# Performance work log

Measured on AMD Instinct MI355X. Metric: run time of the kernel, lower is better.

Reference implementation:

```python
import jax, jax.numpy as jnp
import numpy as np

NUM_NODES = 100000
EMBED_DIM = 128
NUM_RELATIONS = 64
BATCH = 512


def setup_inputs() -> dict:
    key = jax.random.key(0)
    k1, k2, k3, k4, k5 = jax.random.split(key, 5)
    u = jax.random.randint(k1, (BATCH,), 0, NUM_NODES)
    v = jax.random.randint(k2, (BATCH,), 0, NUM_NODES)
    r = jax.random.randint(k3, (BATCH,), 0, NUM_RELATIONS)
    node_embeddings = jax.random.normal(k4, (NUM_NODES, EMBED_DIM), dtype=jnp.float32)
    relation_matrices = jax.random.normal(k5, (NUM_RELATIONS, EMBED_DIM, EMBED_DIM), dtype=jnp.float32)
    return {"u": u, "v": v, "r": r,
            "node_embeddings": node_embeddings,
            "relation_matrices": relation_matrices}


def reference(u, v, r, node_embeddings, relation_matrices):
    u_embed = node_embeddings[u]            # [B, D]
    v_embed = node_embeddings[v]            # [B, D]
    rel = relation_matrices[r]              # [B, D, D] per-sample gathered matrices
    # torch.matmul([B,D], [B,D,D]) broadcasts u_embed over the relation batch -> [B_rel, B_u, D]
    score = jnp.einsum('ud,bde->bue', u_embed, rel)   # [B, B, D]
    # matmul with v_embed.T [D, B] -> [B, B, B]
    score = jnp.einsum('bue,ve->buv', score, v_embed)  # [B, B, B]
    return jax.nn.sigmoid(score)
```

## Files before the change

kernel.cpp:

```cpp
#include <hip/hip_runtime.h>


#define BATCH 512
#define DIM   128
#define NRELS 64
#define NTHR  256

typedef float floatx4 __attribute__((ext_vector_type(4)));

__device__ __forceinline__ void lds_barrier() {
    asm volatile("s_waitcnt lgkmcnt(0)" ::: "memory");
    __builtin_amdgcn_s_barrier();
    __builtin_amdgcn_sched_barrier(0);
}

__global__ __launch_bounds__(NTHR, 2)
void rad_fused_kernel(const int* __restrict__ u_idx,
                      const int* __restrict__ v_idx,
                      const int* __restrict__ r_idx,
                      const float* __restrict__ nodes,
                      const float* __restrict__ rels,
                      float* __restrict__ out)
{
    const int bid = (int)blockIdx.x;
    const int rel = ((bid & 7) << 3) | (bid >> 6);
    const int ut0 = ((bid >> 3) & 7) * 64;

    __shared__ int s_match[BATCH];
    __shared__ int s_mc;
    __shared__ __align__(16) float s_TsT[DIM * 64];
    __shared__ __align__(16) float s_buf[DIM * 64 + 16 * DIM];

    const int t  = (int)threadIdx.x;
    const int tu = t >> 4;
    const int tx = t & 15;

    if (t == 0) s_mc = 0;
    __syncthreads();
    for (int i = t; i < BATCH; i += NTHR) {
        if (r_idx[i] == rel) {
            int p = atomicAdd(&s_mc, 1);
            s_match[p] = i;
        }
    }

    float* UEsT = s_buf;
    float* Rs   = s_buf + DIM * 64;

    for (int i = t; i < 64 * (DIM / 4); i += NTHR) {
        const int row = i & 63;
        const int dc  = i >> 6;
        const float4 val = *reinterpret_cast<const float4*>(
            nodes + (size_t)u_idx[ut0 + row] * DIM + dc * 4);
        UEsT[(dc * 4 + 0) * 64 + row] = val.x;
        UEsT[(dc * 4 + 1) * 64 + row] = val.y;
        UEsT[(dc * 4 + 2) * 64 + row] = val.z;
        UEsT[(dc * 4 + 3) * 64 + row] = val.w;
    }
    __syncthreads();
    const int mc = s_mc;
    if (mc == 0) return;

    float accA[4][8];
    #pragma unroll
    for (int i = 0; i < 4; ++i)
        #pragma unroll
        for (int j = 0; j < 8; ++j) accA[i][j] = 0.f;

    const float* Rbase = rels + (size_t)rel * DIM * DIM;
    for (int dch = 0; dch < DIM / 16; ++dch) {
        for (int i = t; i < 16 * (DIM / 4); i += NTHR) {
            const int rr = i >> 5;
            const int cc = i & 31;
            *reinterpret_cast<float4*>(Rs + rr * DIM + cc * 4) =
                *reinterpret_cast<const float4*>(
                    Rbase + (size_t)(dch * 16 + rr) * DIM + cc * 4);
        }
        lds_barrier();
        #pragma unroll
        for (int dd = 0; dd < 16; ++dd) {
            const int d = dch * 16 + dd;
            const float4 a  = *reinterpret_cast<const float4*>(UEsT + d * 64 + tu * 4);
            const float4 b0 = *reinterpret_cast<const float4*>(Rs + dd * DIM + tx * 4);
            const float4 b1 = *reinterpret_cast<const float4*>(Rs + dd * DIM + 64 + tx * 4);
            const float av[4] = {a.x, a.y, a.z, a.w};
            const float bv[8] = {b0.x, b0.y, b0.z, b0.w, b1.x, b1.y, b1.z, b1.w};
            #pragma unroll
            for (int i = 0; i < 4; ++i)
                #pragma unroll
                for (int j = 0; j < 8; ++j)
                    accA[i][j] = fmaf(av[i], bv[j], accA[i][j]);
        }
        lds_barrier();
    }

    #pragma unroll
    for (int j = 0; j < 8; ++j) {
        const int e = (j < 4) ? (tx * 4 + j) : (64 + tx * 4 + (j - 4));
        #pragma unroll
        for (int i = 0; i < 4; ++i)
            s_TsT[e * 64 + tu * 4 + i] = accA[i][j];
    }

    float* VEsT = s_buf;
    for (int vt = 0; vt < BATCH / 64; ++vt) {
        lds_barrier();
        for (int i = t; i < 64 * (DIM / 4); i += NTHR) {
            const int row = i & 63;
            const int ec  = i >> 6;
            const float4 val = *reinterpret_cast<const float4*>(
                nodes + (size_t)v_idx[vt * 64 + row] * DIM + ec * 4);
            VEsT[(ec * 4 + 0) * 64 + row] = val.x;
            VEsT[(ec * 4 + 1) * 64 + row] = val.y;
            VEsT[(ec * 4 + 2) * 64 + row] = val.z;
            VEsT[(ec * 4 + 3) * 64 + row] = val.w;
        }
        lds_barrier();

        float acc[4][4];
        #pragma unroll
        for (int i = 0; i < 4; ++i)
            #pragma unroll
            for (int j = 0; j < 4; ++j) acc[i][j] = 0.f;

        #pragma unroll 8
        for (int e = 0; e < DIM; ++e) {
            const float4 a = *reinterpret_cast<const float4*>(s_TsT + e * 64 + tu * 4);
            const float4 b = *reinterpret_cast<const float4*>(VEsT  + e * 64 + tx * 4);
            const float av[4] = {a.x, a.y, a.z, a.w};
            const float bv[4] = {b.x, b.y, b.z, b.w};
            #pragma unroll
            for (int i = 0; i < 4; ++i)
                #pragma unroll
                for (int j = 0; j < 4; ++j)
                    acc[i][j] = fmaf(av[i], bv[j], acc[i][j]);
        }

        floatx4 sg[4];
        #pragma unroll
        for (int i = 0; i < 4; ++i) {
            sg[i].x = 1.f / (1.f + __expf(-acc[i][0]));
            sg[i].y = 1.f / (1.f + __expf(-acc[i][1]));
            sg[i].z = 1.f / (1.f + __expf(-acc[i][2]));
            sg[i].w = 1.f / (1.f + __expf(-acc[i][3]));
        }

        for (int m = 0; m < mc; ++m) {
            const int bb = s_match[m];
            float* obase = out + (size_t)bb * BATCH * BATCH + vt * 64 + tx * 4;
            #pragma unroll
            for (int i = 0; i < 4; ++i) {
                __builtin_nontemporal_store(
                    sg[i], reinterpret_cast<floatx4*>(
                               obase + (size_t)(ut0 + tu * 4 + i) * BATCH));
            }
        }
    }
}

extern "C" void kernel_launch(void* const* d_in, const int* in_sizes, int n_in,
                              void* d_out, int out_size, void* d_ws, size_t ws_size,
                              hipStream_t stream) {
    const int*   u_idx = (const int*)d_in[0];
    const int*   v_idx = (const int*)d_in[1];
    const int*   r_idx = (const int*)d_in[2];
    const float* nodes = (const float*)d_in[3];
    const float* rels  = (const float*)d_in[4];
    float* out = (float*)d_out;

    dim3 grid(NRELS * 8);
    dim3 block(NTHR);
    rad_fused_kernel<<<grid, block, 0, stream>>>(u_idx, v_idx, r_idx, nodes, rels, out);
}
```

Before: 142.7 us.

## Widen second-stage tile to 64x256 per block with chunked V staging

The second GEMM stage now processes two 256-wide v halves instead of eight 64-wide tiles. Each thread computes a 16x4 output tile, with the V embeddings staged in 16-column chunks. Each wave's output stores cover 16 full rows of 256 contiguous floats, which should give wider, better-coalesced writes to the large output. This also cuts the number of V reload passes. In exchange it uses a larger accumulator (64 registers), which may pressure occupancy at 2 blocks per CU, and adds more barriers per e-chunk.

```diff
diff --git a/kernel.cpp b/kernel.cpp
--- a/kernel.cpp
+++ b/kernel.cpp
@@ -15,12 +15,12 @@
 }
 
 __global__ __launch_bounds__(NTHR, 2)
-void rad_fused_kernel(const int* __restrict__ u_idx,
-                      const int* __restrict__ v_idx,
-                      const int* __restrict__ r_idx,
-                      const float* __restrict__ nodes,
-                      const float* __restrict__ rels,
-                      float* __restrict__ out)
+void rad_wide_kernel(const int* __restrict__ u_idx,
+                     const int* __restrict__ v_idx,
+                     const int* __restrict__ r_idx,
+                     const float* __restrict__ nodes,
+                     const float* __restrict__ rels,
+                     float* __restrict__ out)
 {
     const int bid = (int)blockIdx.x;
     const int rel = ((bid & 7) << 3) | (bid >> 6);
@@ -28,8 +28,8 @@
 
     __shared__ int s_match[BATCH];
     __shared__ int s_mc;
-    __shared__ __align__(16) float s_TsT[DIM * 64];
-    __shared__ __align__(16) float s_buf[DIM * 64 + 16 * DIM];
+    __shared__ __align__(16) float TsT[DIM * 64];
+    __shared__ __align__(16) float buf[DIM * 64 + 16 * DIM];
 
     const int t  = (int)threadIdx.x;
     const int tu = t >> 4;
@@ -44,8 +44,8 @@
         }
     }
 
-    float* UEsT = s_buf;
-    float* Rs   = s_buf + DIM * 64;
+    float* UEsT = buf;
+    float* Rs   = buf + DIM * 64;
 
     for (int i = t; i < 64 * (DIM / 4); i += NTHR) {
         const int row = i & 63;
@@ -99,60 +99,75 @@
         const int e = (j < 4) ? (tx * 4 + j) : (64 + tx * 4 + (j - 4));
         #pragma unroll
         for (int i = 0; i < 4; ++i)
-            s_TsT[e * 64 + tu * 4 + i] = accA[i][j];
+            TsT[e * 64 + tu * 4 + i] = accA[i][j];
     }
 
-    float* VEsT = s_buf;
-    for (int vt = 0; vt < BATCH / 64; ++vt) {
-        lds_barrier();
-        for (int i = t; i < 64 * (DIM / 4); i += NTHR) {
-            const int row = i & 63;
-            const int ec  = i >> 6;
-            const float4 val = *reinterpret_cast<const float4*>(
-                nodes + (size_t)v_idx[vt * 64 + row] * DIM + ec * 4);
-            VEsT[(ec * 4 + 0) * 64 + row] = val.x;
-            VEsT[(ec * 4 + 1) * 64 + row] = val.y;
-            VEsT[(ec * 4 + 2) * 64 + row] = val.z;
-            VEsT[(ec * 4 + 3) * 64 + row] = val.w;
-        }
-        lds_barrier();
+    const int w  = t >> 6;
+    const int rt = w * 16;
+    const int ct = (t & 63) * 4;
+    float* VEs = buf;
 
-        float acc[4][4];
+    for (int vh = 0; vh < 2; ++vh) {
+        float acc[16][4];
         #pragma unroll
-        for (int i = 0; i < 4; ++i)
+        for (int r = 0; r < 16; ++r)
             #pragma unroll
-            for (int j = 0; j < 4; ++j) acc[i][j] = 0.f;
+            for (int c = 0; c < 4; ++c) acc[r][c] = 0.f;
 
-        #pragma unroll 8
-        for (int e = 0; e < DIM; ++e) {
-            const float4 a = *reinterpret_cast<const float4*>(s_TsT + e * 64 + tu * 4);
-            const float4 b = *reinterpret_cast<const float4*>(VEsT  + e * 64 + tx * 4);
-            const float av[4] = {a.x, a.y, a.z, a.w};
-            const float bv[4] = {b.x, b.y, b.z, b.w};
+        for (int ec = 0; ec < 8; ++ec) {
+            lds_barrier();
             #pragma unroll
-            for (int i = 0; i < 4; ++i)
+            for (int k = 0; k < 4; ++k) {
+                const int i  = t + k * NTHR;
+                const int v  = i & 255;
+                const int c4 = i >> 8;
+                const float4 val = *reinterpret_cast<const float4*>(
+                    nodes + (size_t)v_idx[vh * 256 + v] * DIM + ec * 16 + c4 * 4);
+                VEs[(c4 * 4 + 0) * 256 + v] = val.x;
+                VEs[(c4 * 4 + 1) * 256 + v] = val.y;
+                VEs[(c4 * 4 + 2) * 256 + v] = val.z;
+                VEs[(c4 * 4 + 3) * 256 + v] = val.w;
+            }
+            lds_barrier();
+
+            #pragma unroll 2
+            for (int ee = 0; ee < 16; ++ee) {
+                const int e = ec * 16 + ee;
+                const float4 t0 = *reinterpret_cast<const float4*>(TsT + e * 64 + rt);
+                const float4 t1 = *reinterpret_cast<const float4*>(TsT + e * 64 + rt + 4);
+                const float4 t2 = *reinterpret_cast<const float4*>(TsT + e * 64 + rt + 8);
+                const float4 t3 = *reinterpret_cast<const float4*>(TsT + e * 64 + rt + 12);
+                const float4 bv = *reinterpret_cast<const float4*>(VEs + ee * 256 + ct);
+                const float tr[16] = {t0.x, t0.y, t0.z, t0.w,
+                                      t1.x, t1.y, t1.z, t1.w,
+                                      t2.x, t2.y, t2.z, t2.w,
+                                      t3.x, t3.y, t3.z, t3.w};
+                const float bc[4] = {bv.x, bv.y, bv.z, bv.w};
                 #pragma unroll
-                for (int j = 0; j < 4; ++j)
-                    acc[i][j] = fmaf(av[i], bv[j], acc[i][j]);
+                for (int r = 0; r < 16; ++r)
+                    #pragma unroll
+                    for (int c = 0; c < 4; ++c)
+                        acc[r][c] = fmaf(tr[r], bc[c], acc[r][c]);
+            }
         }
 
-        floatx4 sg[4];
+        floatx4 sg[16];
         #pragma unroll
-        for (int i = 0; i < 4; ++i) {
-            sg[i].x = 1.f / (1.f + __expf(-acc[i][0]));
-            sg[i].y = 1.f / (1.f + __expf(-acc[i][1]));
-            sg[i].z = 1.f / (1.f + __expf(-acc[i][2]));
-            sg[i].w = 1.f / (1.f + __expf(-acc[i][3]));
+        for (int r = 0; r < 16; ++r) {
+            sg[r].x = 1.f / (1.f + __expf(-acc[r][0]));
+            sg[r].y = 1.f / (1.f + __expf(-acc[r][1]));
+            sg[r].z = 1.f / (1.f + __expf(-acc[r][2]));
+            sg[r].w = 1.f / (1.f + __expf(-acc[r][3]));
         }
 
         for (int m = 0; m < mc; ++m) {
             const int bb = s_match[m];
-            float* obase = out + (size_t)bb * BATCH * BATCH + vt * 64 + tx * 4;
+            float* obase = out + ((size_t)bb << 18)
+                               + ((size_t)(ut0 + rt) << 9) + vh * 256 + ct;
             #pragma unroll
-            for (int i = 0; i < 4; ++i) {
+            for (int r = 0; r < 16; ++r) {
                 __builtin_nontemporal_store(
-                    sg[i], reinterpret_cast<floatx4*>(
-                               obase + (size_t)(ut0 + tu * 4 + i) * BATCH));
+                    sg[r], reinterpret_cast<floatx4*>(obase + ((size_t)r << 9)));
             }
         }
     }
@@ -170,5 +185,5 @@
 
     dim3 grid(NRELS * 8);
     dim3 block(NTHR);
-    rad_fused_kernel<<<grid, block, 0, stream>>>(u_idx, v_idx, r_idx, nodes, rels, out);
+    rad_wide_kernel<<<grid, block, 0, stream>>>(u_idx, v_idx, r_idx, nodes, rels, out);
 }
```

Measured after the change: 152.9 us. 1.07x slower.
